# Kernel optimization log

Measured on AMD Instinct MI355X. Metric: run time of the kernel, lower is better.

## Reference

```python
import jax, jax.numpy as jnp
import numpy as np


def _rbf_forward(batches, centers, beta, W, b):
    # Pairwise Euclidean distances via GEMM expansion instead of materializing
    # the O(n*K*dim) difference tensor the torch code builds.
    x2 = jnp.sum(batches * batches, axis=1, keepdims=True)          # [n, 1]
    c2 = jnp.sum(centers * centers, axis=1)                          # [K]
    xc = jnp.einsum('nd,kd->nk', batches, centers)                   # [n, K]
    d2 = jnp.maximum(x2 + c2[None, :] - 2.0 * xc, 0.0)               # [n, K]
    dist = jnp.sqrt(d2)
    radial = jnp.exp(-beta * dist)                                   # beta: [1, K]
    return radial @ W.T + b                                          # [n, num_class]


def setup_inputs() -> dict:
    key = jax.random.key(0)
    k1, k2, k3, k4, k5 = jax.random.split(key, 5)
    n, K, dim, num_class = 16384, 2048, 512, 10
    batches = jax.random.normal(k1, (n, dim), dtype=jnp.float32)
    centers = jax.random.normal(k2, (K, dim), dtype=jnp.float32)
    beta = jnp.full((1, K), 0.1, dtype=jnp.float32)  # torch init: ones/10
    W = jax.random.normal(k4, (num_class, K), dtype=jnp.float32) / np.sqrt(K)
    b = jax.random.normal(k5, (num_class,), dtype=jnp.float32) * 0.01
    return {"batches": batches, "centers": centers, "beta": beta, "W": W, "b": b}


def reference(batches, centers, beta, W, b):
    return _rbf_forward(batches, centers, beta, W, b)
```

## Files before the change

kernel.cpp:

```cpp
#include <hip/hip_runtime.h>
#include <hip/hip_bf16.h>
#include <stdint.h>

#define M_N  16384
#define K_C  2048
#define DIM  512
#define NCLS 10
#define NBN  16
#define NBM  (M_N / 128)

typedef unsigned short u16;
typedef float  f32x4  __attribute__((ext_vector_type(4)));
typedef __bf16 bf16x8 __attribute__((ext_vector_type(8)));


__device__ __forceinline__ void async_ld16(const void* g, void* l) {
  __builtin_amdgcn_global_load_lds(
      (const __attribute__((address_space(1))) void*)g,
      (__attribute__((address_space(3))) void*)l,
      16, 0, 0);
}

__device__ __forceinline__ u16 f2bf_rne(float f) {
  uint32_t u = __float_as_uint(f);
  u += 0x7FFFu + ((u >> 16) & 1u);
  return (u16)(u >> 16);
}


#define NPREP ((M_N + K_C) / 2)

__global__ __launch_bounds__(256) void prep(
    const float4* __restrict__ batches, const float4* __restrict__ centers,
    const float* __restrict__ W,
    ushort4* __restrict__ Abf, ushort4* __restrict__ Bbf,
    float* __restrict__ x2, float* __restrict__ c2, u16* __restrict__ Wperm) {
  int b = blockIdx.x, t = threadIdx.x;
  if (b < NPREP) {
    int rp = b * 2 + (t >> 7);
    int col = t & 127;
    const float4* src; ushort4* dst; float* sq; int row;
    if (rp < M_N) { src = batches; dst = Abf; sq = x2; row = rp; }
    else          { src = centers; dst = Bbf; sq = c2; row = rp - M_N; }
    float4 v = src[(size_t)row * 128 + col];
    float ss = v.x * v.x + v.y * v.y + v.z * v.z + v.w * v.w;
    ushort4 o;
    o.x = f2bf_rne(v.x); o.y = f2bf_rne(v.y);
    o.z = f2bf_rne(v.z); o.w = f2bf_rne(v.w);
    dst[(size_t)row * 128 + col] = o;
    ss += __shfl_down(ss, 32);
    ss += __shfl_down(ss, 16);
    ss += __shfl_down(ss, 8);
    ss += __shfl_down(ss, 4);
    ss += __shfl_down(ss, 2);
    ss += __shfl_down(ss, 1);
    __shared__ float part[4];
    if ((t & 63) == 0) part[t >> 6] = ss;
    __syncthreads();
    if (t == 0) sq[row] = part[0] + part[1];
    if (t == 128) sq[row] = part[2] + part[3];
  } else {
    int wb = b - NPREP;
#pragma unroll
    for (int i = 0; i < 4; ++i) {
      int p = wb * 1024 + i * 256 + t;
      int cls = p >> 11, k = p & 2047;
      int bn = k >> 7, rem = k & 127;
      int hh = (rem >> 6) & 1, tt = (rem >> 5) & 1;
      int qq = (rem >> 3) & 3, jj = rem & 7;
      int c = bn * 128 + hh * 64 + (tt * 2 + (jj >> 2)) * 16 + qq * 4 + (jj & 3);
      Wperm[p] = (cls < NCLS) ? f2bf_rne(W[cls * K_C + c]) : (u16)0;
    }
  }
}


__global__ __launch_bounds__(256, 4) void rbf_main(
    const u16* __restrict__ A,
    const u16* __restrict__ B,
    const float* __restrict__ x2,
    const float* __restrict__ c2,
    const float* __restrict__ beta,
    const u16* __restrict__ Wperm,
    float* __restrict__ partial) {
  constexpr int BK = 64;
  __shared__ alignas(16) unsigned char smem[32768];
  u16* As = (u16*)smem;
  u16* Bs = (u16*)(smem + 16384);
  f32x4* sumbuf = (f32x4*)smem;

  const int tid  = threadIdx.x;
  const int lane = tid & 63;
  const int wid  = tid >> 6;
  const int bid = blockIdx.x;
  const int g = bid >> 3, r8 = bid & 7;
  const int bm = r8 * 16 + (g & 15);
  const int bn = g >> 4;
  const int row0 = bm * 128, col0 = bn * 128;
  const int wrC = (wid >> 1) * 64;
  const int wcB = (wid & 1) * 64;

  f32x4 acc[4][4] = {};

  const int srow = tid >> 3;
  const int scol = ((tid & 7) ^ (srow & 7)) * 8;
  const u16* aG = A + (size_t)(row0 + srow) * DIM + scol;
  const u16* bG = B + (size_t)(col0 + srow) * DIM + scol;
  u16* aL = As + tid * 8;
  u16* bL = Bs + tid * 8;

  const int frow = lane & 15;
  const int fq   = lane >> 4;
  const int fsw  = frow & 7;

  for (int k0 = 0; k0 < DIM; k0 += BK) {
    __syncthreads();
#pragma unroll
    for (int i = 0; i < 4; ++i) {
      async_ld16(aG + k0 + i * 32 * DIM, aL + i * 2048);
      async_ld16(bG + k0 + i * 32 * DIM, bL + i * 2048);
    }
    __syncthreads();

#pragma unroll
    for (int kh = 0; kh < 2; ++kh) {
      const int slot = ((kh << 2) | fq) ^ fsw;
      bf16x8 cf[4], bfr[4];
#pragma unroll
      for (int mi = 0; mi < 4; ++mi)
        cf[mi] = *(const bf16x8*)(Bs + (wrC + mi * 16 + frow) * BK + slot * 8);
#pragma unroll
      for (int ni = 0; ni < 4; ++ni)
        bfr[ni] = *(const bf16x8*)(As + (wcB + ni * 16 + frow) * BK + slot * 8);
#pragma unroll
      for (int mi = 0; mi < 4; ++mi)
#pragma unroll
        for (int ni = 0; ni < 4; ++ni)
          acc[mi][ni] = __builtin_amdgcn_mfma_f32_16x16x32_bf16(
              cf[mi], bfr[ni], acc[mi][ni], 0, 0, 0);
    }
  }

  const int cls = lane & 15, q = lane >> 4;
  float4 c2q[4], btq[4];
#pragma unroll
  for (int mi = 0; mi < 4; ++mi) {
    int base = col0 + wrC + mi * 16 + q * 4;
    c2q[mi] = *(const float4*)(c2 + base);
    btq[mi] = *(const float4*)(beta + base);
  }
  float x2v[4];
#pragma unroll
  for (int ni = 0; ni < 4; ++ni)
    x2v[ni] = x2[row0 + wcB + ni * 16 + cls];

#pragma unroll
  for (int mi = 0; mi < 4; ++mi)
#pragma unroll
    for (int ni = 0; ni < 4; ++ni)
#pragma unroll
      for (int r = 0; r < 4; ++r) {
        float xc = acc[mi][ni][r];
        float d2 = fmaxf(x2v[ni] + c2q[mi][r] - 2.0f * xc, 0.0f);
        acc[mi][ni][r] = __expf(-btq[mi][r] * sqrtf(d2));
      }

  const int h = wid >> 1;
  bf16x8 wfr[2];
#pragma unroll
  for (int t = 0; t < 2; ++t)
    wfr[t] = *(const bf16x8*)(Wperm + (size_t)cls * K_C + col0 + h * 64 +
                              t * 32 + q * 8);

  f32x4 acc2[4] = {};
#pragma unroll
  for (int ni = 0; ni < 4; ++ni) {
#pragma unroll
    for (int t = 0; t < 2; ++t) {
      union { u16 hh[8]; bf16x8 v; } pk;
#pragma unroll
      for (int r = 0; r < 4; ++r) {
        pk.hh[r]     = f2bf_rne(acc[2 * t][ni][r]);
        pk.hh[4 + r] = f2bf_rne(acc[2 * t + 1][ni][r]);
      }
      acc2[ni] = __builtin_amdgcn_mfma_f32_16x16x32_bf16(
          pk.v, wfr[t], acc2[ni], 0, 0, 0);
    }
  }

  __syncthreads();
  if (wid >= 2) {
#pragma unroll
    for (int ni = 0; ni < 4; ++ni)
      sumbuf[((wid & 1) * 4 + ni) * 64 + lane] = acc2[ni];
  }
  __syncthreads();
  if (wid < 2) {
#pragma unroll
    for (int ni = 0; ni < 4; ++ni) {
      f32x4 o = sumbuf[(wid * 4 + ni) * 64 + lane];
      acc2[ni] += o;
#pragma unroll
      for (int r = 0; r < 4; ++r) {
        int gr = row0 + wid * 64 + ni * 16 + q * 4 + r;
        __builtin_nontemporal_store(
            acc2[ni][r], &partial[((size_t)bn * M_N + gr) * 16 + cls]);
      }
    }
  }
}


__global__ __launch_bounds__(256) void reduce_out(
    const float* __restrict__ partial, const float* __restrict__ b,
    float* __restrict__ out) {
  int t = threadIdx.x;
  int row = blockIdx.x * 64 + (t >> 2);
  int quad = t & 3;
  f32x4 v = {0.f, 0.f, 0.f, 0.f};
#pragma unroll
  for (int bn = 0; bn < NBN; ++bn) {
    f32x4 p = __builtin_nontemporal_load(
        (const f32x4*)(partial + ((size_t)bn * M_N + row) * 16 + quad * 4));
    v += p;
  }
  if (quad == 0) {
    float4 bq = *(const float4*)b;
    float* o = out + (size_t)row * NCLS;
    *(float2*)o       = {v.x + bq.x, v.y + bq.y};
    *(float2*)(o + 2) = {v.z + bq.z, v.w + bq.w};
  } else if (quad == 1) {
    float4 bq = *(const float4*)(b + 4);
    float* o = out + (size_t)row * NCLS + 4;
    *(float2*)o       = {v.x + bq.x, v.y + bq.y};
    *(float2*)(o + 2) = {v.z + bq.z, v.w + bq.w};
  } else if (quad == 2) {
    *(float2*)(out + (size_t)row * NCLS + 8) = {v.x + b[8], v.y + b[9]};
  }
}


extern "C" void kernel_launch(void* const* d_in, const int* in_sizes, int n_in,
                              void* d_out, int out_size, void* d_ws, size_t ws_size,
                              hipStream_t stream) {
  const float* batches = (const float*)d_in[0];
  const float* centers = (const float*)d_in[1];
  const float* beta    = (const float*)d_in[2];
  const float* W       = (const float*)d_in[3];
  const float* bias    = (const float*)d_in[4];
  float* out = (float*)d_out;

  char* ws = (char*)d_ws;
  u16*  Abf = (u16*)ws;
  u16*  Bbf = (u16*)(ws + (size_t)M_N * DIM * 2);
  float* x2 = (float*)(ws + (size_t)(M_N + K_C) * DIM * 2);
  float* c2 = x2 + M_N;
  u16*  Wpm = (u16*)(c2 + K_C);
  float* partial = (float*)((char*)Wpm + 16 * K_C * 2);

  prep<<<dim3(NPREP + 32), dim3(256), 0, stream>>>(
      (const float4*)batches, (const float4*)centers, W,
      (ushort4*)Abf, (ushort4*)Bbf, x2, c2, Wpm);
  rbf_main<<<dim3(NBN * NBM), dim3(256), 0, stream>>>(
      Abf, Bbf, x2, c2, beta, Wpm, partial);
  reduce_out<<<dim3(M_N / 64), dim3(256), 0, stream>>>(partial, bias, out);
}
```

Measured before the change: 136.5 us.

## Widen GEMM tile to 128x256, double-buffer B in LDS, load A from global

The main kernel tile grows to 128 rows by 256 centers, with each wave owning 128 centers by 64 rows (32 accumulators). Center tiles are now double-buffered in LDS with async loads so the next K-slice is fetched while the current one is computed. Batch operands are read directly from global memory into registers instead of staged through LDS. The cross-wave LDS reduction is replaced by writing 16 partial slices, and prep switches to one wave per row so it no longer needs a barrier. The cost is higher register pressure (launch bound drops to 2 blocks) and uncoalesced, cache-dependent global reads for A.

```diff
diff --git a/kernel.cpp b/kernel.cpp
--- a/kernel.cpp
+++ b/kernel.cpp
@@ -6,8 +6,10 @@
 #define K_C  2048
 #define DIM  512
 #define NCLS 10
-#define NBN  16
-#define NBM  (M_N / 128)
+#define NSL  16
+#define BM   128
+#define BN   256
+#define BK   64
 
 typedef unsigned short u16;
 typedef float  f32x4  __attribute__((ext_vector_type(4)));
@@ -28,7 +30,7 @@
 }
 
 
-#define NPREP ((M_N + K_C) / 2)
+#define NPREP ((M_N + K_C) / 4)
 
 __global__ __launch_bounds__(256) void prep(
     const float4* __restrict__ batches, const float4* __restrict__ centers,
@@ -37,45 +39,45 @@
     float* __restrict__ x2, float* __restrict__ c2, u16* __restrict__ Wperm) {
   int b = blockIdx.x, t = threadIdx.x;
   if (b < NPREP) {
-    int rp = b * 2 + (t >> 7);
-    int col = t & 127;
+    int lane = t & 63;
+    int rp = b * 4 + (t >> 6);
     const float4* src; ushort4* dst; float* sq; int row;
     if (rp < M_N) { src = batches; dst = Abf; sq = x2; row = rp; }
     else          { src = centers; dst = Bbf; sq = c2; row = rp - M_N; }
-    float4 v = src[(size_t)row * 128 + col];
-    float ss = v.x * v.x + v.y * v.y + v.z * v.z + v.w * v.w;
-    ushort4 o;
-    o.x = f2bf_rne(v.x); o.y = f2bf_rne(v.y);
-    o.z = f2bf_rne(v.z); o.w = f2bf_rne(v.w);
-    dst[(size_t)row * 128 + col] = o;
+    float ss = 0.f;
+#pragma unroll
+    for (int i = 0; i < 2; ++i) {
+      float4 v = src[(size_t)row * 128 + i * 64 + lane];
+      ss += v.x * v.x + v.y * v.y + v.z * v.z + v.w * v.w;
+      ushort4 o;
+      o.x = f2bf_rne(v.x); o.y = f2bf_rne(v.y);
+      o.z = f2bf_rne(v.z); o.w = f2bf_rne(v.w);
+      dst[(size_t)row * 128 + i * 64 + lane] = o;
+    }
     ss += __shfl_down(ss, 32);
     ss += __shfl_down(ss, 16);
     ss += __shfl_down(ss, 8);
     ss += __shfl_down(ss, 4);
     ss += __shfl_down(ss, 2);
     ss += __shfl_down(ss, 1);
-    __shared__ float part[4];
-    if ((t & 63) == 0) part[t >> 6] = ss;
-    __syncthreads();
-    if (t == 0) sq[row] = part[0] + part[1];
-    if (t == 128) sq[row] = part[2] + part[3];
+    if (lane == 0) sq[row] = ss;
   } else {
     int wb = b - NPREP;
 #pragma unroll
     for (int i = 0; i < 4; ++i) {
       int p = wb * 1024 + i * 256 + t;
       int cls = p >> 11, k = p & 2047;
-      int bn = k >> 7, rem = k & 127;
-      int hh = (rem >> 6) & 1, tt = (rem >> 5) & 1;
-      int qq = (rem >> 3) & 3, jj = rem & 7;
-      int c = bn * 128 + hh * 64 + (tt * 2 + (jj >> 2)) * 16 + qq * 4 + (jj & 3);
+      int bnn = k >> 8, rem = k & 255;
+      int h = rem >> 7, rem2 = rem & 127;
+      int tt = rem2 >> 5, qq = (rem2 >> 3) & 3, jj = rem2 & 7;
+      int c = bnn * 256 + h * 128 + (2 * tt + (jj >> 2)) * 16 + qq * 4 + (jj & 3);
       Wperm[p] = (cls < NCLS) ? f2bf_rne(W[cls * K_C + c]) : (u16)0;
     }
   }
 }
 
 
-__global__ __launch_bounds__(256, 4) void rbf_main(
+__global__ __launch_bounds__(256, 2) void rbf_main(
     const u16* __restrict__ A,
     const u16* __restrict__ B,
     const float* __restrict__ x2,
@@ -83,11 +85,7 @@
     const float* __restrict__ beta,
     const u16* __restrict__ Wperm,
     float* __restrict__ partial) {
-  constexpr int BK = 64;
-  __shared__ alignas(16) unsigned char smem[32768];
-  u16* As = (u16*)smem;
-  u16* Bs = (u16*)(smem + 16384);
-  f32x4* sumbuf = (f32x4*)smem;
+  __shared__ u16 Bs[2][BN * BK];
 
   const int tid  = threadIdx.x;
   const int lane = tid & 63;
@@ -96,87 +94,84 @@
   const int g = bid >> 3, r8 = bid & 7;
   const int bm = r8 * 16 + (g & 15);
   const int bn = g >> 4;
-  const int row0 = bm * 128, col0 = bn * 128;
-  const int wrC = (wid >> 1) * 64;
-  const int wcB = (wid & 1) * 64;
-
-  f32x4 acc[4][4] = {};
+  const int row0 = bm * BM, col0 = bn * BN;
+  const int wc2 = (wid & 1) * 128;
+  const int wb2 = (wid >> 1) * 64;
+  const int cls = lane & 15, q = lane >> 4;
+  const int fsw = cls & 7;
+
+  f32x4 acc[8][4] = {};
 
   const int srow = tid >> 3;
-  const int scol = ((tid & 7) ^ (srow & 7)) * 8;
-  const u16* aG = A + (size_t)(row0 + srow) * DIM + scol;
-  const u16* bG = B + (size_t)(col0 + srow) * DIM + scol;
-  u16* aL = As + tid * 8;
-  u16* bL = Bs + tid * 8;
-
-  const int frow = lane & 15;
-  const int fq   = lane >> 4;
-  const int fsw  = frow & 7;
-
-  for (int k0 = 0; k0 < DIM; k0 += BK) {
+  const int schunk = (tid & 7) ^ (srow & 7);
+  const u16* bG = B + (size_t)(col0 + srow) * DIM + schunk * 8;
+
+  const u16* aR[4];
+#pragma unroll
+  for (int ni = 0; ni < 4; ++ni)
+    aR[ni] = A + (size_t)(row0 + wb2 + ni * 16 + cls) * DIM + q * 8;
+
+#define FILL(buf, k0)                                                    \
+  {                                                                      \
+    _Pragma("unroll")                                                    \
+    for (int i = 0; i < 8; ++i)                                          \
+      async_ld16(bG + (k0) + i * 32 * DIM, &Bs[buf][i * 2048] + tid * 8);\
+  }
+
+  FILL(0, 0)
+  for (int it = 0; it < 8; ++it) {
     __syncthreads();
-#pragma unroll
-    for (int i = 0; i < 4; ++i) {
-      async_ld16(aG + k0 + i * 32 * DIM, aL + i * 2048);
-      async_ld16(bG + k0 + i * 32 * DIM, bL + i * 2048);
-    }
-    __syncthreads();
-
+    if (it < 7) FILL((it + 1) & 1, (it + 1) * BK)
+    const u16* bsb = Bs[it & 1];
+    bf16x8 bfr[2][4];
+#pragma unroll
+    for (int kh = 0; kh < 2; ++kh)
+#pragma unroll
+      for (int ni = 0; ni < 4; ++ni)
+        bfr[kh][ni] = *(const bf16x8*)(aR[ni] + it * BK + kh * 32);
 #pragma unroll
     for (int kh = 0; kh < 2; ++kh) {
-      const int slot = ((kh << 2) | fq) ^ fsw;
-      bf16x8 cf[4], bfr[4];
-#pragma unroll
-      for (int mi = 0; mi < 4; ++mi)
-        cf[mi] = *(const bf16x8*)(Bs + (wrC + mi * 16 + frow) * BK + slot * 8);
-#pragma unroll
-      for (int ni = 0; ni < 4; ++ni)
-        bfr[ni] = *(const bf16x8*)(As + (wcB + ni * 16 + frow) * BK + slot * 8);
-#pragma unroll
-      for (int mi = 0; mi < 4; ++mi)
+      bf16x8 cf[8];
+#pragma unroll
+      for (int mi = 0; mi < 8; ++mi)
+        cf[mi] = *(const bf16x8*)(bsb + (wc2 + mi * 16 + cls) * BK +
+                                  (((kh << 2) | q) ^ fsw) * 8);
+#pragma unroll
+      for (int mi = 0; mi < 8; ++mi)
 #pragma unroll
         for (int ni = 0; ni < 4; ++ni)
           acc[mi][ni] = __builtin_amdgcn_mfma_f32_16x16x32_bf16(
-              cf[mi], bfr[ni], acc[mi][ni], 0, 0, 0);
-    }
-  }
-
-  const int cls = lane & 15, q = lane >> 4;
-  float4 c2q[4], btq[4];
-#pragma unroll
-  for (int mi = 0; mi < 4; ++mi) {
-    int base = col0 + wrC + mi * 16 + q * 4;
-    c2q[mi] = *(const float4*)(c2 + base);
-    btq[mi] = *(const float4*)(beta + base);
-  }
+              cf[mi], bfr[kh][ni], acc[mi][ni], 0, 0, 0);
+    }
+  }
+
   float x2v[4];
 #pragma unroll
   for (int ni = 0; ni < 4; ++ni)
-    x2v[ni] = x2[row0 + wcB + ni * 16 + cls];
-
-#pragma unroll
-  for (int mi = 0; mi < 4; ++mi)
+    x2v[ni] = x2[row0 + wb2 + ni * 16 + cls];
+#pragma unroll
+  for (int mi = 0; mi < 8; ++mi) {
+    int base = col0 + wc2 + mi * 16 + q * 4;
+    float4 cq = *(const float4*)(c2 + base);
+    float4 bq = *(const float4*)(beta + base);
 #pragma unroll
     for (int ni = 0; ni < 4; ++ni)
 #pragma unroll
       for (int r = 0; r < 4; ++r) {
         float xc = acc[mi][ni][r];
-        float d2 = fmaxf(x2v[ni] + c2q[mi][r] - 2.0f * xc, 0.0f);
-        acc[mi][ni][r] = __expf(-btq[mi][r] * sqrtf(d2));
+        float d2 = fmaxf(x2v[ni] + cq[r] - 2.0f * xc, 0.0f);
+        acc[mi][ni][r] = __expf(-bq[r] * sqrtf(d2));
       }
-
-  const int h = wid >> 1;
-  bf16x8 wfr[2];
-#pragma unroll
-  for (int t = 0; t < 2; ++t)
-    wfr[t] = *(const bf16x8*)(Wperm + (size_t)cls * K_C + col0 + h * 64 +
-                              t * 32 + q * 8);
-
+  }
+
+  const int h = wid & 1;
   f32x4 acc2[4] = {};
 #pragma unroll
-  for (int ni = 0; ni < 4; ++ni) {
-#pragma unroll
-    for (int t = 0; t < 2; ++t) {
+  for (int t = 0; t < 4; ++t) {
+    bf16x8 wfr = *(const bf16x8*)(Wperm + (size_t)cls * K_C + col0 +
+                                  h * 128 + t * 32 + q * 8);
+#pragma unroll
+    for (int ni = 0; ni < 4; ++ni) {
       union { u16 hh[8]; bf16x8 v; } pk;
 #pragma unroll
       for (int r = 0; r < 4; ++r) {
@@ -184,30 +179,19 @@
         pk.hh[4 + r] = f2bf_rne(acc[2 * t + 1][ni][r]);
       }
       acc2[ni] = __builtin_amdgcn_mfma_f32_16x16x32_bf16(
-          pk.v, wfr[t], acc2[ni], 0, 0, 0);
-    }
-  }
-
-  __syncthreads();
-  if (wid >= 2) {
-#pragma unroll
-    for (int ni = 0; ni < 4; ++ni)
-      sumbuf[((wid & 1) * 4 + ni) * 64 + lane] = acc2[ni];
-  }
-  __syncthreads();
-  if (wid < 2) {
-#pragma unroll
-    for (int ni = 0; ni < 4; ++ni) {
-      f32x4 o = sumbuf[(wid * 4 + ni) * 64 + lane];
-      acc2[ni] += o;
-#pragma unroll
-      for (int r = 0; r < 4; ++r) {
-        int gr = row0 + wid * 64 + ni * 16 + q * 4 + r;
-        __builtin_nontemporal_store(
-            acc2[ni][r], &partial[((size_t)bn * M_N + gr) * 16 + cls]);
-      }
-    }
-  }
+          pk.v, wfr, acc2[ni], 0, 0, 0);
+    }
+  }
+
+  const int slice = bn * 2 + h;
+#pragma unroll
+  for (int ni = 0; ni < 4; ++ni)
+#pragma unroll
+    for (int r = 0; r < 4; ++r) {
+      int gr = row0 + wb2 + ni * 16 + q * 4 + r;
+      __builtin_nontemporal_store(
+          acc2[ni][r], &partial[((size_t)slice * M_N + gr) * 16 + cls]);
+    }
 }
 
 
@@ -219,9 +203,9 @@
   int quad = t & 3;
   f32x4 v = {0.f, 0.f, 0.f, 0.f};
 #pragma unroll
-  for (int bn = 0; bn < NBN; ++bn) {
+  for (int s = 0; s < NSL; ++s) {
     f32x4 p = __builtin_nontemporal_load(
-        (const f32x4*)(partial + ((size_t)bn * M_N + row) * 16 + quad * 4));
+        (const f32x4*)(partial + ((size_t)s * M_N + row) * 16 + quad * 4));
     v += p;
   }
   if (quad == 0) {
@@ -261,7 +245,7 @@
   prep<<<dim3(NPREP + 32), dim3(256), 0, stream>>>(
       (const float4*)batches, (const float4*)centers, W,
       (ushort4*)Abf, (ushort4*)Bbf, x2, c2, Wpm);
-  rbf_main<<<dim3(NBN * NBM), dim3(256), 0, stream>>>(
+  rbf_main<<<dim3(8 * (M_N / BM)), dim3(256), 0, stream>>>(
       Abf, Bbf, x2, c2, beta, Wpm, partial);
   reduce_out<<<dim3(M_N / 64), dim3(256), 0, stream>>>(partial, bias, out);
 }
```

Measured after the change: 162.2 us. +18.9%, slower.

## Double-buffer GEMM K-loop with BK=32 and one-wave-per-row prep kernel

Applied to the files above, without the earlier changes.

The main kernel's K loop now uses two LDS buffers with BK=32. The next tile is prefetched asynchronously while the current one is consumed, which drops one barrier per iteration and overlaps global loads with MFMA work. The swizzle pattern and fragment offsets are recomputed for the narrower tile. The prep kernel now gives each wave a full row, removing the shared-memory reduction and its barrier. Other changes: the bf16 packing uses native casts, and the partial stores are no longer nontemporal. Halving BK doubles the iteration count, so per-iteration sync overhead remains.

```diff
diff --git a/kernel.cpp b/kernel.cpp
--- a/kernel.cpp
+++ b/kernel.cpp
@@ -8,6 +8,7 @@
 #define NCLS 10
 #define NBN  16
 #define NBM  (M_N / 128)
+#define BK   32
 
 typedef unsigned short u16;
 typedef float  f32x4  __attribute__((ext_vector_type(4)));
@@ -28,7 +29,7 @@
 }
 
 
-#define NPREP ((M_N + K_C) / 2)
+#define NPREP ((M_N + K_C) / 4)
 
 __global__ __launch_bounds__(256) void prep(
     const float4* __restrict__ batches, const float4* __restrict__ centers,
@@ -37,28 +38,28 @@
     float* __restrict__ x2, float* __restrict__ c2, u16* __restrict__ Wperm) {
   int b = blockIdx.x, t = threadIdx.x;
   if (b < NPREP) {
-    int rp = b * 2 + (t >> 7);
-    int col = t & 127;
+    int lane = t & 63;
+    int rp = b * 4 + (t >> 6);
     const float4* src; ushort4* dst; float* sq; int row;
     if (rp < M_N) { src = batches; dst = Abf; sq = x2; row = rp; }
     else          { src = centers; dst = Bbf; sq = c2; row = rp - M_N; }
-    float4 v = src[(size_t)row * 128 + col];
-    float ss = v.x * v.x + v.y * v.y + v.z * v.z + v.w * v.w;
-    ushort4 o;
-    o.x = f2bf_rne(v.x); o.y = f2bf_rne(v.y);
-    o.z = f2bf_rne(v.z); o.w = f2bf_rne(v.w);
-    dst[(size_t)row * 128 + col] = o;
+    float ss = 0.f;
+#pragma unroll
+    for (int i = 0; i < 2; ++i) {
+      float4 v = src[(size_t)row * 128 + i * 64 + lane];
+      ss += v.x * v.x + v.y * v.y + v.z * v.z + v.w * v.w;
+      ushort4 o;
+      o.x = f2bf_rne(v.x); o.y = f2bf_rne(v.y);
+      o.z = f2bf_rne(v.z); o.w = f2bf_rne(v.w);
+      dst[(size_t)row * 128 + i * 64 + lane] = o;
+    }
     ss += __shfl_down(ss, 32);
     ss += __shfl_down(ss, 16);
     ss += __shfl_down(ss, 8);
     ss += __shfl_down(ss, 4);
     ss += __shfl_down(ss, 2);
     ss += __shfl_down(ss, 1);
-    __shared__ float part[4];
-    if ((t & 63) == 0) part[t >> 6] = ss;
-    __syncthreads();
-    if (t == 0) sq[row] = part[0] + part[1];
-    if (t == 128) sq[row] = part[2] + part[3];
+    if (lane == 0) sq[row] = ss;
   } else {
     int wb = b - NPREP;
 #pragma unroll
@@ -66,9 +67,9 @@
       int p = wb * 1024 + i * 256 + t;
       int cls = p >> 11, k = p & 2047;
       int bn = k >> 7, rem = k & 127;
-      int hh = (rem >> 6) & 1, tt = (rem >> 5) & 1;
-      int qq = (rem >> 3) & 3, jj = rem & 7;
-      int c = bn * 128 + hh * 64 + (tt * 2 + (jj >> 2)) * 16 + qq * 4 + (jj & 3);
+      int h = (rem >> 6) & 1, rem2 = rem & 63;
+      int tt = rem2 >> 5, qq = (rem2 >> 3) & 3, jj = rem2 & 7;
+      int c = bn * 128 + h * 64 + (2 * tt + (jj >> 2)) * 16 + qq * 4 + (jj & 3);
       Wperm[p] = (cls < NCLS) ? f2bf_rne(W[cls * K_C + c]) : (u16)0;
     }
   }
@@ -83,11 +84,8 @@
     const float* __restrict__ beta,
     const u16* __restrict__ Wperm,
     float* __restrict__ partial) {
-  constexpr int BK = 64;
-  __shared__ alignas(16) unsigned char smem[32768];
-  u16* As = (u16*)smem;
-  u16* Bs = (u16*)(smem + 16384);
-  f32x4* sumbuf = (f32x4*)smem;
+  __shared__ alignas(16) u16 As[2][128 * BK];
+  __shared__ alignas(16) u16 Bs[2][128 * BK];
 
   const int tid  = threadIdx.x;
   const int lane = tid & 63;
@@ -99,112 +97,107 @@
   const int row0 = bm * 128, col0 = bn * 128;
   const int wrC = (wid >> 1) * 64;
   const int wcB = (wid & 1) * 64;
+  const int cls = lane & 15, q = lane >> 4;
 
   f32x4 acc[4][4] = {};
 
-  const int srow = tid >> 3;
-  const int scol = ((tid & 7) ^ (srow & 7)) * 8;
-  const u16* aG = A + (size_t)(row0 + srow) * DIM + scol;
-  const u16* bG = B + (size_t)(col0 + srow) * DIM + scol;
-  u16* aL = As + tid * 8;
-  u16* bL = Bs + tid * 8;
-
-  const int frow = lane & 15;
-  const int fq   = lane >> 4;
-  const int fsw  = frow & 7;
-
-  for (int k0 = 0; k0 < DIM; k0 += BK) {
+  const int srow = tid >> 2;
+  const int schunk = (tid & 3) ^ ((tid >> 3) & 3);
+  const u16* aG = A + (size_t)(row0 + srow) * DIM + schunk * 8;
+  const u16* bG = B + (size_t)(col0 + srow) * DIM + schunk * 8;
+
+#define FILL(buf, k0)                                          \
+  {                                                            \
+    async_ld16(aG + (k0),            &As[buf][0]    + tid * 8);\
+    async_ld16(aG + (k0) + 64 * DIM, &As[buf][2048] + tid * 8);\
+    async_ld16(bG + (k0),            &Bs[buf][0]    + tid * 8);\
+    async_ld16(bG + (k0) + 64 * DIM, &Bs[buf][2048] + tid * 8);\
+  }
+
+  int offC[4], offB[4];
+#pragma unroll
+  for (int i = 0; i < 4; ++i) {
+    int rrC = wrC + i * 16 + cls;
+    offC[i] = rrC * BK + (q ^ ((rrC >> 1) & 3)) * 8;
+    int rrB = wcB + i * 16 + cls;
+    offB[i] = rrB * BK + (q ^ ((rrB >> 1) & 3)) * 8;
+  }
+
+  FILL(0, 0)
+  for (int it = 0; it < 16; ++it) {
     __syncthreads();
-#pragma unroll
-    for (int i = 0; i < 4; ++i) {
-      async_ld16(aG + k0 + i * 32 * DIM, aL + i * 2048);
-      async_ld16(bG + k0 + i * 32 * DIM, bL + i * 2048);
-    }
-    __syncthreads();
-
-#pragma unroll
-    for (int kh = 0; kh < 2; ++kh) {
-      const int slot = ((kh << 2) | fq) ^ fsw;
-      bf16x8 cf[4], bfr[4];
-#pragma unroll
-      for (int mi = 0; mi < 4; ++mi)
-        cf[mi] = *(const bf16x8*)(Bs + (wrC + mi * 16 + frow) * BK + slot * 8);
+    if (it < 15) FILL((it + 1) & 1, (it + 1) * BK)
+    const u16* as_ = As[it & 1];
+    const u16* bs_ = Bs[it & 1];
+    bf16x8 cf[4], bfr[4];
+#pragma unroll
+    for (int mi = 0; mi < 4; ++mi)
+      cf[mi] = *(const bf16x8*)(bs_ + offC[mi]);
+#pragma unroll
+    for (int ni = 0; ni < 4; ++ni)
+      bfr[ni] = *(const bf16x8*)(as_ + offB[ni]);
+#pragma unroll
+    for (int mi = 0; mi < 4; ++mi)
 #pragma unroll
       for (int ni = 0; ni < 4; ++ni)
-        bfr[ni] = *(const bf16x8*)(As + (wcB + ni * 16 + frow) * BK + slot * 8);
-#pragma unroll
-      for (int mi = 0; mi < 4; ++mi)
-#pragma unroll
-        for (int ni = 0; ni < 4; ++ni)
-          acc[mi][ni] = __builtin_amdgcn_mfma_f32_16x16x32_bf16(
-              cf[mi], bfr[ni], acc[mi][ni], 0, 0, 0);
-    }
-  }
-
-  const int cls = lane & 15, q = lane >> 4;
-  float4 c2q[4], btq[4];
+        acc[mi][ni] = __builtin_amdgcn_mfma_f32_16x16x32_bf16(
+            cf[mi], bfr[ni], acc[mi][ni], 0, 0, 0);
+  }
+
+  float x2v[4];
+#pragma unroll
+  for (int ni = 0; ni < 4; ++ni)
+    x2v[ni] = x2[row0 + wcB + ni * 16 + cls];
 #pragma unroll
   for (int mi = 0; mi < 4; ++mi) {
     int base = col0 + wrC + mi * 16 + q * 4;
-    c2q[mi] = *(const float4*)(c2 + base);
-    btq[mi] = *(const float4*)(beta + base);
-  }
-  float x2v[4];
-#pragma unroll
-  for (int ni = 0; ni < 4; ++ni)
-    x2v[ni] = x2[row0 + wcB + ni * 16 + cls];
-
-#pragma unroll
-  for (int mi = 0; mi < 4; ++mi)
+    float4 cq = *(const float4*)(c2 + base);
+    float4 bq = *(const float4*)(beta + base);
 #pragma unroll
     for (int ni = 0; ni < 4; ++ni)
 #pragma unroll
       for (int r = 0; r < 4; ++r) {
         float xc = acc[mi][ni][r];
-        float d2 = fmaxf(x2v[ni] + c2q[mi][r] - 2.0f * xc, 0.0f);
-        acc[mi][ni][r] = __expf(-btq[mi][r] * sqrtf(d2));
+        float d2 = fmaxf(x2v[ni] + cq[r] - 2.0f * xc, 0.0f);
+        acc[mi][ni][r] = __expf(-bq[r] * sqrtf(d2));
       }
+  }
 
   const int h = wid >> 1;
-  bf16x8 wfr[2];
-#pragma unroll
-  for (int t = 0; t < 2; ++t)
-    wfr[t] = *(const bf16x8*)(Wperm + (size_t)cls * K_C + col0 + h * 64 +
-                              t * 32 + q * 8);
-
   f32x4 acc2[4] = {};
 #pragma unroll
-  for (int ni = 0; ni < 4; ++ni) {
-#pragma unroll
-    for (int t = 0; t < 2; ++t) {
-      union { u16 hh[8]; bf16x8 v; } pk;
+  for (int t = 0; t < 2; ++t) {
+    bf16x8 wfr = *(const bf16x8*)(Wperm + (size_t)cls * K_C + col0 +
+                                  h * 64 + t * 32 + q * 8);
+#pragma unroll
+    for (int ni = 0; ni < 4; ++ni) {
+      bf16x8 pk;
 #pragma unroll
       for (int r = 0; r < 4; ++r) {
-        pk.hh[r]     = f2bf_rne(acc[2 * t][ni][r]);
-        pk.hh[4 + r] = f2bf_rne(acc[2 * t + 1][ni][r]);
+        pk[r]     = (__bf16)acc[2 * t][ni][r];
+        pk[4 + r] = (__bf16)acc[2 * t + 1][ni][r];
       }
       acc2[ni] = __builtin_amdgcn_mfma_f32_16x16x32_bf16(
-          pk.v, wfr[t], acc2[ni], 0, 0, 0);
-    }
-  }
-
+          pk, wfr, acc2[ni], 0, 0, 0);
+    }
+  }
+
+  f32x4* sumbuf = (f32x4*)As;
   __syncthreads();
   if (wid >= 2) {
 #pragma unroll
     for (int ni = 0; ni < 4; ++ni)
-      sumbuf[((wid & 1) * 4 + ni) * 64 + lane] = acc2[ni];
+      sumbuf[((wid - 2) * 4 + ni) * 64 + lane] = acc2[ni];
   }
   __syncthreads();
   if (wid < 2) {
 #pragma unroll
     for (int ni = 0; ni < 4; ++ni) {
-      f32x4 o = sumbuf[(wid * 4 + ni) * 64 + lane];
-      acc2[ni] += o;
+      acc2[ni] += sumbuf[(wid * 4 + ni) * 64 + lane];
 #pragma unroll
       for (int r = 0; r < 4; ++r) {
         int gr = row0 + wid * 64 + ni * 16 + q * 4 + r;
-        __builtin_nontemporal_store(
-            acc2[ni][r], &partial[((size_t)bn * M_N + gr) * 16 + cls]);
+        partial[((size_t)bn * M_N + gr) * 16 + cls] = acc2[ni][r];
       }
     }
   }
@@ -219,9 +212,9 @@
   int quad = t & 3;
   f32x4 v = {0.f, 0.f, 0.f, 0.f};
 #pragma unroll
-  for (int bn = 0; bn < NBN; ++bn) {
+  for (int s = 0; s < NBN; ++s) {
     f32x4 p = __builtin_nontemporal_load(
-        (const f32x4*)(partial + ((size_t)bn * M_N + row) * 16 + quad * 4));
+        (const f32x4*)(partial + ((size_t)s * M_N + row) * 16 + quad * 4));
     v += p;
   }
   if (quad == 0) {
```

Result: no change. 137.3 us (+0.6%).
